# Performance work log

Hardware: AMD Instinct MI355X
Metric: run time of the kernel (lower is better)

The kernel has to match this reference:

```python
import jax, jax.numpy as jnp
import numpy as np

B, S, D = 4, 4096, 256

def setup_inputs() -> dict:
    key = jax.random.key(0)
    k1, k2, k3, k4 = jax.random.split(key, 4)
    inputs = jax.random.normal(k1, (B, S, D), dtype=jnp.float32)
    Wq = jax.random.normal(k2, (D, D), dtype=jnp.float32) * 0.05
    Wk = jax.random.normal(k3, (D, D), dtype=jnp.float32) * 0.05
    Wv = jax.random.normal(k4, (D, D), dtype=jnp.float32) * 0.05
    return {"inputs": inputs, "Wq": Wq, "Wk": Wk, "Wv": Wv}

def reference(inputs, Wq, Wk, Wv):
    # single-head self-attention: softmax(QK^T / sqrt(d)) V
    d = inputs.shape[-1]
    Q = jnp.einsum('bsd,de->bse', inputs, Wq)
    K = jnp.einsum('bsd,de->bse', inputs, Wk)
    V = jnp.einsum('bsd,de->bse', inputs, Wv)
    scale = 1.0 / jnp.sqrt(jnp.asarray(d, dtype=inputs.dtype))
    scores = jnp.einsum('bqe,bke->bqk', Q, K) * scale  # [B,S,S]
    attn = jax.nn.softmax(scores, axis=-1)
    return jnp.einsum('bqk,bke->bqe', attn, V)
```

## Files before the change

kernel.cpp:

```cpp
#include <hip/hip_runtime.h>
#include <hip/hip_bf16.h>

typedef __attribute__((ext_vector_type(8))) short bfrag_t;
typedef __attribute__((ext_vector_type(4))) short s4_t;
typedef __attribute__((ext_vector_type(4))) float facc_t;
typedef __attribute__((ext_vector_type(16))) float f16acc_t;
typedef __attribute__((ext_vector_type(4))) int i4_t;

#define B_ 4
#define S_ 4096
#define D_ 256

using gas_v = const __attribute__((address_space(1))) void;
using las_v = __attribute__((address_space(3))) void;

__device__ __forceinline__ short f2bf(float f) {
  union { float fv; unsigned u; } x; x.fv = f;
  unsigned r = x.u + 0x7FFFu + ((x.u >> 16) & 1u);
  return (short)(r >> 16);
}

__device__ __forceinline__ int cvtpk(float lo, float hi) {
  int r;
  asm("v_cvt_pk_bf16_f32 %0, %1, %2" : "=v"(r) : "v"(lo), "v"(hi));
  return r;
}

__device__ __forceinline__ float fexp2(float x) {
  float r;
  asm("v_exp_f32 %0, %1" : "=v"(r) : "v"(x));
  return r;
}

__device__ __forceinline__ facc_t mfma16(bfrag_t a, bfrag_t b, facc_t c) {
  return __builtin_amdgcn_mfma_f32_16x16x32_bf16(a, b, c, 0, 0, 0);
}
__device__ __forceinline__ f16acc_t mfma32(bfrag_t a, bfrag_t b, f16acc_t c) {
  return __builtin_amdgcn_mfma_f32_32x32x16_bf16(a, b, c, 0, 0, 0);
}

__global__ __launch_bounds__(256) void wt_kernel(
    const float* __restrict__ Wq, const float* __restrict__ Wk,
    const float* __restrict__ Wv, short* __restrict__ WT) {
  __shared__ short Tl[256 * 68];
  const int p = blockIdx.x >> 2;
  const int estripe = (blockIdx.x & 3) * 64;
  const float* W = (p == 0) ? Wq : ((p == 1) ? Wk : Wv);
  short* o = WT + p * (D_ * D_);
  const int el = threadIdx.x & 63, dq = threadIdx.x >> 6;
  #pragma unroll 16
  for (int pass = 0; pass < 64; ++pass) {
    int d = pass * 4 + dq;
    Tl[d * 68 + el] = f2bf(W[d * 256 + estripe + el]);
  }
  __syncthreads();
  const int eo = threadIdx.x >> 2, qd = threadIdx.x & 3;
  #pragma unroll
  for (int j = 0; j < 8; ++j) {
    s4_t a, b2;
    #pragma unroll
    for (int t2 = 0; t2 < 4; ++t2) a[t2]  = Tl[(qd * 64 + j * 8 + t2) * 68 + eo];
    #pragma unroll
    for (int t2 = 0; t2 < 4; ++t2) b2[t2] = Tl[(qd * 64 + j * 8 + 4 + t2) * 68 + eo];
    short* dst = o + (estripe + eo) * 256 + qd * 64 + j * 8;
    *reinterpret_cast<s4_t*>(dst) = a;
    *reinterpret_cast<s4_t*>(dst + 4) = b2;
  }
}

__global__ __launch_bounds__(256) void proj_kernel(
    const float* __restrict__ X, const short* __restrict__ WT,
    short* __restrict__ Qb, short* __restrict__ Kb, short* __restrict__ VT) {
  __shared__ __align__(16) short Stg[256 * 72];
  const int tid  = threadIdx.x;
  const int wave = tid >> 6, lane = tid & 63;
  const int lrow = lane & 15, kch = lane >> 4;
  const int p  = blockIdx.x >> 8;
  const int rb = blockIdx.x & 255;
  const int row0 = rb * 64 + wave * 16;
  const int arow = row0 + lrow;
  const int bblk = rb >> 6;

  bfrag_t af[8];
  #pragma unroll
  for (int kt = 0; kt < 8; ++kt) {
    const float* src = X + (size_t)arow * D_ + kt * 32 + kch * 8;
    float4 a = *reinterpret_cast<const float4*>(src);
    float4 b = *reinterpret_cast<const float4*>(src + 4);
    bfrag_t f;
    f[0] = f2bf(a.x); f[1] = f2bf(a.y); f[2] = f2bf(a.z); f[3] = f2bf(a.w);
    f[4] = f2bf(b.x); f[5] = f2bf(b.y); f[6] = f2bf(b.z); f[7] = f2bf(b.w);
    af[kt] = f;
  }

  const short* Wp = WT + p * (D_ * D_);
  facc_t acc[16];
  #pragma unroll
  for (int nt = 0; nt < 16; ++nt) acc[nt] = (facc_t)0.0f;
  #pragma unroll
  for (int kt = 0; kt < 8; ++kt) {
    #pragma unroll
    for (int nt = 0; nt < 16; ++nt) {
      bfrag_t bf = *reinterpret_cast<const bfrag_t*>(
          Wp + (nt * 16 + lrow) * D_ + kt * 32 + kch * 8);
      acc[nt] = mfma16(af[kt], bf, acc[nt]);
    }
  }
  if (p < 2) {
    const float sc = (p == 0) ? 0.09016844f : 1.0f;
    #pragma unroll
    for (int nt = 0; nt < 16; ++nt)
      #pragma unroll
      for (int r = 0; r < 4; ++r)
        Stg[(wave * 16 + kch * 4 + r) * 264 + nt * 16 + lrow] =
            f2bf(acc[nt][r] * sc);
    __syncthreads();
    short* dstbase = ((p == 0) ? Qb : Kb) + (size_t)rb * 64 * D_;
    #pragma unroll
    for (int k = 0; k < 8; ++k) {
      int c = k * 256 + tid;
      int row = c >> 5, col = c & 31;
      *reinterpret_cast<bfrag_t*>(dstbase + row * D_ + col * 8) =
          *reinterpret_cast<const bfrag_t*>(&Stg[row * 264 + col * 8]);
    }
  } else {
    #pragma unroll
    for (int nt = 0; nt < 16; ++nt) {
      s4_t v;
      #pragma unroll
      for (int r = 0; r < 4; ++r) v[r] = f2bf(acc[nt][r]);
      *reinterpret_cast<s4_t*>(
          &Stg[(nt * 16 + lrow) * 72 + (wave >> 1) * 32 + (wave & 1) * 16 +
               (kch & 1) * 8 + (kch >> 1) * 4]) = v;
    }
    __syncthreads();
    const int d = tid;
    const int s0 = (rb & 63) * 64;
    short* dst = VT + ((size_t)(bblk * D_ + d)) * S_ + s0;
    #pragma unroll
    for (int j = 0; j < 8; ++j)
      *reinterpret_cast<bfrag_t*>(dst + j * 8) =
          *reinterpret_cast<const bfrag_t*>(&Stg[d * 72 + j * 8]);
  }
}

template<int SPLIT>
__global__ __launch_bounds__(256, 2) void attn32(
    const short* __restrict__ Qb, const short* __restrict__ Kb,
    const short* __restrict__ VT, float* __restrict__ P0,
    float* __restrict__ PX, float2* __restrict__ ML) {
  __shared__ __align__(16) short Kl[2][32 * 256];
  __shared__ __align__(16) short Vl[2][256 * 32];
  const int tid  = threadIdx.x;
  const int wave = tid >> 6, lane = tid & 63;
  const int l31 = lane & 31, hi = lane >> 5;
  const int ksw = (lane & 7) << 4;
  const int vsw = ((l31 >> 1) & 3) << 4;
  const int hw = blockIdx.x;
  const int g = hw & 7, rest = hw >> 3;
  int b, part, qblk;
  if constexpr (SPLIT == 4)      { b = g >> 1; part = (g & 1) * 2 + (rest & 1); qblk = rest >> 1; }
  else if constexpr (SPLIT == 2) { b = g >> 1; part = g & 1;                    qblk = rest; }
  else                           { b = g >> 1; part = 0;                qblk = (g & 1) * 16 + rest; }
  const int q0 = qblk * 128 + wave * 32;
  const int kvbase = part * (S_ / SPLIT);
  constexpr int STEPS = (S_ / SPLIT) / 32;

  const short* Kbp = Kb + (size_t)b * S_ * D_ + (size_t)kvbase * D_;
  const short* Vbp = VT + (size_t)b * D_ * S_ + kvbase;

  bfrag_t qf[16];
  const short* Qp = Qb + ((size_t)b * S_ + q0 + l31) * D_;
  #pragma unroll
  for (int kt = 0; kt < 16; ++kt)
    qf[kt] = *reinterpret_cast<const bfrag_t*>(Qp + kt * 16 + hi * 8);

  auto stage = [&](int bf, int kv0) {
    #pragma unroll
    for (int j = 0; j < 4; ++j) {
      int L = j * 4096 + tid * 16;
      int row = L >> 9;
      int cs = (L & 511) ^ ((row & 7) << 4);
      const short* src = Kbp + (size_t)(kv0 + row) * D_ + (cs >> 1);
      short* dst = &Kl[bf][(j * 4096 + wave * 1024) >> 1];
      __builtin_amdgcn_global_load_lds((gas_v*)src, (las_v*)dst, 16, 0, 0);
    }
    #pragma unroll
    for (int j = 0; j < 4; ++j) {
      int L = j * 4096 + tid * 16;
      int d = L >> 6;
      int cs = (L & 63) ^ (((d >> 1) & 3) << 4);
      const short* src = Vbp + (size_t)d * S_ + kv0 + (cs >> 1);
      short* dst = &Vl[bf][(j * 4096 + wave * 1024) >> 1];
      __builtin_amdgcn_global_load_lds((gas_v*)src, (las_v*)dst, 16, 0, 0);
    }
  };

  f16acc_t o32[8];
  #pragma unroll
  for (int nt = 0; nt < 8; ++nt) o32[nt] = (f16acc_t)0.0f;
  float mrow = -3.0e38f, lsum = 0.0f;

  stage(0, 0);
  asm volatile("s_waitcnt vmcnt(0)" ::: "memory");
  __syncthreads();
  int buf = 0;

  #pragma unroll 1
  for (int t = 0; t < STEPS; ++t) {
    if (t < STEPS - 1) stage(buf ^ 1, (t + 1) * 32);
    f16acc_t s16 = (f16acc_t)0.0f;
    const char* Kbase = (const char*)&Kl[buf][0];
    __builtin_amdgcn_s_setprio(1);
    #pragma unroll
    for (int kt = 0; kt < 16; ++kt) {
      bfrag_t kf = *reinterpret_cast<const bfrag_t*>(
          Kbase + l31 * 512 + ((kt * 32 + hi * 16) ^ ksw));
      s16 = mfma32(kf, qf[kt], s16);
    }
    __builtin_amdgcn_s_setprio(0);
    float a0 = fmaxf(fmaxf(s16[0], s16[1]), s16[2]);
    float a1 = fmaxf(fmaxf(s16[3], s16[4]), s16[5]);
    float a2 = fmaxf(fmaxf(s16[6], s16[7]), s16[8]);
    float a3 = fmaxf(fmaxf(s16[9], s16[10]), s16[11]);
    float a4 = fmaxf(fmaxf(s16[12], s16[13]), s16[14]);
    float b0 = fmaxf(fmaxf(a0, a1), a2);
    float b1 = fmaxf(fmaxf(a3, a4), s16[15]);
    float mx = fmaxf(b0, b1);
    mx = fmaxf(mx, __shfl_xor(mx, 32));
    if (mx > mrow + 11.0f) {
      float sf = fexp2(mrow - mx);
      mrow = mx;
      lsum *= sf;
      #pragma unroll
      for (int nt = 0; nt < 8; ++nt) o32[nt] *= sf;
    }
    float pe[16];
    float ls = 0.0f;
    #pragma unroll
    for (int i = 0; i < 16; ++i) {
      pe[i] = fexp2(s16[i] - mrow);
      ls += pe[i];
    }
    lsum += ls;
    i4_t w0, w1;
    w0.x = cvtpk(pe[0], pe[1]);  w0.y = cvtpk(pe[2], pe[3]);
    w0.z = cvtpk(pe[4], pe[5]);  w0.w = cvtpk(pe[6], pe[7]);
    w1.x = cvtpk(pe[8], pe[9]);  w1.y = cvtpk(pe[10], pe[11]);
    w1.z = cvtpk(pe[12], pe[13]); w1.w = cvtpk(pe[14], pe[15]);
    bfrag_t pb0 = __builtin_bit_cast(bfrag_t, w0);
    bfrag_t pb1 = __builtin_bit_cast(bfrag_t, w1);
    const char* Vbase = (const char*)&Vl[buf][0];
    __builtin_amdgcn_s_setprio(1);
    #pragma unroll
    for (int nt = 0; nt < 8; ++nt) {
      const char* vb = Vbase + (nt * 32 + l31) * 64;
      bfrag_t v0 = *reinterpret_cast<const bfrag_t*>(vb + ((hi * 16) ^ vsw));
      o32[nt] = mfma32(v0, pb0, o32[nt]);
      bfrag_t v1 = *reinterpret_cast<const bfrag_t*>(vb + ((32 + hi * 16) ^ vsw));
      o32[nt] = mfma32(v1, pb1, o32[nt]);
    }
    __builtin_amdgcn_s_setprio(0);
    asm volatile("s_waitcnt vmcnt(0)" ::: "memory");
    __syncthreads();
    buf ^= 1;
  }

  lsum += __shfl_xor(lsum, 32);
  float* Pd = (SPLIT == 1 || part == 0)
                  ? P0 : PX + (size_t)(part - 1) * ((size_t)B_ * S_ * D_);
  float* Og = Pd + ((size_t)b * S_ + q0 + l31) * D_;
  if constexpr (SPLIT == 1) {
    float inv = 1.0f / lsum;
    #pragma unroll
    for (int nt = 0; nt < 8; ++nt)
      #pragma unroll
      for (int gg = 0; gg < 4; ++gg) {
        float4 o;
        o.x = o32[nt][gg * 4 + 0] * inv; o.y = o32[nt][gg * 4 + 1] * inv;
        o.z = o32[nt][gg * 4 + 2] * inv; o.w = o32[nt][gg * 4 + 3] * inv;
        *reinterpret_cast<float4*>(Og + nt * 32 + hi * 4 + gg * 8) = o;
      }
  } else {
    #pragma unroll
    for (int nt = 0; nt < 8; ++nt)
      #pragma unroll
      for (int gg = 0; gg < 4; ++gg) {
        float4 o;
        o.x = o32[nt][gg * 4 + 0]; o.y = o32[nt][gg * 4 + 1];
        o.z = o32[nt][gg * 4 + 2]; o.w = o32[nt][gg * 4 + 3];
        *reinterpret_cast<float4*>(Og + nt * 32 + hi * 4 + gg * 8) = o;
      }
    if (lane < 32) {
      float2 ml; ml.x = mrow; ml.y = lsum;
      ML[part * (B_ * S_) + b * S_ + q0 + l31] = ml;
    }
  }
}

template<int SPLIT>
__global__ __launch_bounds__(256) void combineN(
    const float* __restrict__ PX, const float2* __restrict__ ML,
    float* __restrict__ Out) {
  const int r = blockIdx.x * 4 + (threadIdx.x >> 6);
  const int d4 = (threadIdx.x & 63) * 4;
  float2 ml[SPLIT];
  #pragma unroll
  for (int p = 0; p < SPLIT; ++p) ml[p] = ML[p * (B_ * S_) + r];
  float m = ml[0].x;
  #pragma unroll
  for (int p = 1; p < SPLIT; ++p) m = fmaxf(m, ml[p].x);
  float w[SPLIT];
  float denom = 0.0f;
  #pragma unroll
  for (int p = 0; p < SPLIT; ++p) {
    w[p] = fexp2(ml[p].x - m);
    denom += ml[p].y * w[p];
  }
  float inv = 1.0f / denom;
  size_t idx = (size_t)r * D_ + d4;
  float4 x = *reinterpret_cast<float4*>(Out + idx);
  float4 acc;
  acc.x = x.x * w[0]; acc.y = x.y * w[0]; acc.z = x.z * w[0]; acc.w = x.w * w[0];
  #pragma unroll
  for (int p = 1; p < SPLIT; ++p) {
    float4 y = *reinterpret_cast<const float4*>(
        PX + (size_t)(p - 1) * ((size_t)B_ * S_ * D_) + idx);
    acc.x += y.x * w[p]; acc.y += y.y * w[p];
    acc.z += y.z * w[p]; acc.w += y.w * w[p];
  }
  acc.x *= inv; acc.y *= inv; acc.z *= inv; acc.w *= inv;
  *reinterpret_cast<float4*>(Out + idx) = acc;
}

extern "C" void kernel_launch(void* const* d_in, const int* in_sizes, int n_in,
                              void* d_out, int out_size, void* d_ws, size_t ws_size,
                              hipStream_t stream) {
  const float* X  = (const float*)d_in[0];
  const float* Wq = (const float*)d_in[1];
  const float* Wk = (const float*)d_in[2];
  const float* Wv = (const float*)d_in[3];
  float* out = (float*)d_out;

  char* ws = (char*)d_ws;
  short* Qb = (short*)(ws);
  short* Kb = (short*)(ws + 8388608);
  short* VT = (short*)(ws + 16777216);
  short* WT = (short*)(ws + 25165824);
  float2* ML = (float2*)(ws + 25690112);
  float* PX  = (float*)(ws + 26214400);
  const size_t NP = (size_t)B_ * S_ * D_ * 4;
  const size_t need4 = 26214400 + 3 * NP;
  const size_t need2 = 26214400 + 1 * NP;

  wt_kernel<<<12, 256, 0, stream>>>(Wq, Wk, Wv, WT);
  proj_kernel<<<768, 256, 0, stream>>>(X, WT, Qb, Kb, VT);
  if (ws_size >= need4) {
    attn32<4><<<512, 256, 0, stream>>>(Qb, Kb, VT, out, PX, ML);
    combineN<4><<<(B_ * S_) / 4, 256, 0, stream>>>(PX, ML, out);
  } else if (ws_size >= need2) {
    attn32<2><<<256, 256, 0, stream>>>(Qb, Kb, VT, out, PX, ML);
    combineN<2><<<(B_ * S_) / 4, 256, 0, stream>>>(PX, ML, out);
  } else {
    attn32<1><<<128, 256, 0, stream>>>(Qb, Kb, VT, out, PX, (float2*)out);
  }
}
```

Measured before the change: 158.2 us.

## Fuse split-KV combine into attention kernel via last-block atomic counter

```diff
diff --git a/kernel.cpp b/kernel.cpp
--- a/kernel.cpp
+++ b/kernel.cpp
@@ -148,7 +148,7 @@
 __global__ __launch_bounds__(256, 2) void attn32(
     const short* __restrict__ Qb, const short* __restrict__ Kb,
     const short* __restrict__ VT, float* __restrict__ P0,
-    float* __restrict__ PX, float2* __restrict__ ML) {
+    float* __restrict__ PX, float2* __restrict__ ML, int* __restrict__ cnt) {
   __shared__ __align__(16) short Kl[2][32 * 256];
   __shared__ __align__(16) short Vl[2][256 * 32];
   const int tid  = threadIdx.x;
@@ -159,9 +159,9 @@
   const int hw = blockIdx.x;
   const int g = hw & 7, rest = hw >> 3;
   int b, part, qblk;
-  if constexpr (SPLIT == 4)      { b = g >> 1; part = (g & 1) * 2 + (rest & 1); qblk = rest >> 1; }
-  else if constexpr (SPLIT == 2) { b = g >> 1; part = g & 1;                    qblk = rest; }
-  else                           { b = g >> 1; part = 0;                qblk = (g & 1) * 16 + rest; }
+  if constexpr (SPLIT == 4)      { int combo = ((rest & 1) << 3) | g; b = combo >> 2; part = combo & 3; qblk = rest >> 1; }
+  else if constexpr (SPLIT == 2) { b = g >> 1; part = g & 1;          qblk = rest; }
+  else                           { b = g >> 1; part = 0;              qblk = (g & 1) * 16 + rest; }
   const int q0 = qblk * 128 + wave * 32;
   const int kvbase = part * (S_ / SPLIT);
   constexpr int STEPS = (S_ / SPLIT) / 32;
@@ -244,9 +244,9 @@
     }
     lsum += ls;
     i4_t w0, w1;
-    w0.x = cvtpk(pe[0], pe[1]);  w0.y = cvtpk(pe[2], pe[3]);
-    w0.z = cvtpk(pe[4], pe[5]);  w0.w = cvtpk(pe[6], pe[7]);
-    w1.x = cvtpk(pe[8], pe[9]);  w1.y = cvtpk(pe[10], pe[11]);
+    w0.x = cvtpk(pe[0], pe[1]);   w0.y = cvtpk(pe[2], pe[3]);
+    w0.z = cvtpk(pe[4], pe[5]);   w0.w = cvtpk(pe[6], pe[7]);
+    w1.x = cvtpk(pe[8], pe[9]);   w1.y = cvtpk(pe[10], pe[11]);
     w1.z = cvtpk(pe[12], pe[13]); w1.w = cvtpk(pe[14], pe[15]);
     bfrag_t pb0 = __builtin_bit_cast(bfrag_t, w0);
     bfrag_t pb1 = __builtin_bit_cast(bfrag_t, w1);
@@ -296,6 +296,50 @@
       ML[part * (B_ * S_) + b * S_ + q0 + l31] = ml;
     }
   }
+  if constexpr (SPLIT == 4) {
+    __threadfence();
+    __syncthreads();
+    __shared__ int lastS;
+    if (tid == 0)
+      lastS = (atomicAdd(&cnt[b * 32 + qblk], 1) == SPLIT - 1);
+    __syncthreads();
+    if (lastS) {
+      __threadfence();
+      const size_t NPf = (size_t)B_ * S_ * D_;
+      #pragma unroll 1
+      for (int it = 0; it < 32; ++it) {
+        int grow = b * S_ + qblk * 128 + it * 4 + (tid >> 6);
+        float2 ml[SPLIT];
+        #pragma unroll
+        for (int p = 0; p < SPLIT; ++p) ml[p] = ML[p * (B_ * S_) + grow];
+        float m = ml[0].x;
+        #pragma unroll
+        for (int p = 1; p < SPLIT; ++p) m = fmaxf(m, ml[p].x);
+        float w[SPLIT];
+        float denom = 0.0f;
+        #pragma unroll
+        for (int p = 0; p < SPLIT; ++p) {
+          w[p] = fexp2(ml[p].x - m);
+          denom += ml[p].y * w[p];
+        }
+        float inv = 1.0f / denom;
+        size_t idx = (size_t)grow * D_ + (tid & 63) * 4;
+        float4 x = *reinterpret_cast<const float4*>(P0 + idx);
+        float4 acc;
+        acc.x = x.x * w[0]; acc.y = x.y * w[0];
+        acc.z = x.z * w[0]; acc.w = x.w * w[0];
+        #pragma unroll
+        for (int p = 1; p < SPLIT; ++p) {
+          float4 y = *reinterpret_cast<const float4*>(
+              PX + (size_t)(p - 1) * NPf + idx);
+          acc.x += y.x * w[p]; acc.y += y.y * w[p];
+          acc.z += y.z * w[p]; acc.w += y.w * w[p];
+        }
+        acc.x *= inv; acc.y *= inv; acc.z *= inv; acc.w *= inv;
+        *reinterpret_cast<float4*>(P0 + idx) = acc;
+      }
+    }
+  }
 }
 
 template<int SPLIT>
@@ -347,6 +391,7 @@
   short* Kb = (short*)(ws + 8388608);
   short* VT = (short*)(ws + 16777216);
   short* WT = (short*)(ws + 25165824);
+  int*   CN = (int*)(ws + 25559040);
   float2* ML = (float2*)(ws + 25690112);
   float* PX  = (float*)(ws + 26214400);
   const size_t NP = (size_t)B_ * S_ * D_ * 4;
@@ -356,12 +401,12 @@
   wt_kernel<<<12, 256, 0, stream>>>(Wq, Wk, Wv, WT);
   proj_kernel<<<768, 256, 0, stream>>>(X, WT, Qb, Kb, VT);
   if (ws_size >= need4) {
-    attn32<4><<<512, 256, 0, stream>>>(Qb, Kb, VT, out, PX, ML);
-    combineN<4><<<(B_ * S_) / 4, 256, 0, stream>>>(PX, ML, out);
+    hipMemsetAsync(CN, 0, 512, stream);
+    attn32<4><<<512, 256, 0, stream>>>(Qb, Kb, VT, out, PX, ML, CN);
   } else if (ws_size >= need2) {
-    attn32<2><<<256, 256, 0, stream>>>(Qb, Kb, VT, out, PX, ML);
+    attn32<2><<<256, 256, 0, stream>>>(Qb, Kb, VT, out, PX, ML, CN);
     combineN<2><<<(B_ * S_) / 4, 256, 0, stream>>>(PX, ML, out);
   } else {
-    attn32<1><<<128, 256, 0, stream>>>(Qb, Kb, VT, out, PX, (float2*)out);
-  }
-}
+    attn32<1><<<128, 256, 0, stream>>>(Qb, Kb, VT, out, PX, (float2*)out, CN);
+  }
+}
```

Result: slower. 257.8 us (+63.0%).
